# Performance work log

Hardware: AMD Instinct MI355X
Metric: run time of the kernel (lower is better)

The kernel has to match this reference:

```python
import jax, jax.numpy as jnp
import numpy as np

H = 4        # num_heads
DH = 64      # output_dim (d_head)
D = 256      # input_dim (hidden)
NUM_LAYERS = 2


def _gru_cell(x, h, Wih, Whh, bih, bhh):
    # PyTorch GRUCell: gates ordered (r, z, n)
    gi = x @ Wih.T + bih
    gh = h @ Whh.T + bhh
    i_r, i_z, i_n = jnp.split(gi, 3, axis=-1)
    h_r, h_z, h_n = jnp.split(gh, 3, axis=-1)
    r = jax.nn.sigmoid(i_r + h_r)
    z = jax.nn.sigmoid(i_z + h_z)
    n = jnp.tanh(i_n + r * h_n)
    return (1.0 - z) * n + z * h


def _mha(x, attn_mask, Wq, bq, Wk, bk, Wv, bv, Wo):
    B, N, _ = x.shape
    q = (x @ Wq.T + bq).reshape(B, N, H, DH)
    k = (x @ Wk.T + bk).reshape(B, N, H, DH)
    v = (x @ Wv.T + bv).reshape(B, N, H, DH)
    # scores computed in fp32 (autocast disabled in original)
    scores = jnp.einsum('bnhd,bmhd->bhnm', q.astype(jnp.float32), k.astype(jnp.float32)) / jnp.float32(DH) ** 0.5
    scores = jnp.where(attn_mask[:, None], jnp.float32(-1e9), scores)  # mask broadcast over heads
    attn = jax.nn.softmax(scores, axis=-1)
    ctx = jnp.einsum('bhnm,bmhd->bnhd', attn, v).reshape(B, N, H * DH)
    return ctx @ Wo.T  # W_O has no bias


def setup_inputs() -> dict:
    B, N = 1024, 128
    key = jax.random.key(0)
    ks = jax.random.split(key, 14)
    s = 0.02
    return {
        'latent': jax.random.normal(ks[0], (B, N, D), jnp.float32),
        'comm_mask': jax.random.randint(ks[1], (B, N, N), 0, 2) > 0,
        'trait_weight': jax.random.normal(ks[2], (B, N), jnp.float32),
        'Wq': jax.random.normal(ks[3], (H * DH, D), jnp.float32) * s,
        'bq': jnp.zeros((H * DH,), jnp.float32),
        'Wk': jax.random.normal(ks[4], (H * DH, D), jnp.float32) * s,
        'bk': jnp.zeros((H * DH,), jnp.float32),
        'Wv': jax.random.normal(ks[5], (H * DH, D), jnp.float32) * s,
        'bv': jnp.zeros((H * DH,), jnp.float32),
        'Wo': jax.random.normal(ks[6], (DH, H * DH), jnp.float32) * s,
        'Wih': jax.random.normal(ks[7], (3 * D, DH), jnp.float32) * s,
        'Whh': jax.random.normal(ks[8], (3 * D, D), jnp.float32) * s,
        'bih': jnp.zeros((3 * D,), jnp.float32),
        'bhh': jnp.zeros((3 * D,), jnp.float32),
    }


def reference(latent, comm_mask, trait_weight, Wq, bq, Wk, bk, Wv, bv, Wo, Wih, Whh, bih, bhh):
    B, N, _ = latent.shape
    attn_mask = ~comm_mask                                    # [B,N,N] True = blocked
    update_mask = (comm_mask.sum(axis=-1) > 1)[..., None]     # [B,N,1]
    for _ in range(NUM_LAYERS):
        info = _mha(latent, attn_mask, Wq, bq, Wk, bk, Wv, bv, Wo)          # [B,N,DH]
        upd = _gru_cell(info.reshape(-1, DH), latent.reshape(-1, D), Wih, Whh, bih, bhh)
        latent = jnp.where(update_mask, upd.reshape(B, N, D), latent)
    return latent
```

## Files before the change

kernel.cpp:

```cpp
#include <hip/hip_runtime.h>
#include <stdint.h>

#define NTOK 128
#define DHID 256
#define NHEAD 4
#define DHEAD 64

typedef short bf16x8 __attribute__((ext_vector_type(8)));
typedef float f32x4 __attribute__((ext_vector_type(4)));

#define MFMA(a,b,c) __builtin_amdgcn_mfma_f32_16x16x32_bf16((a),(b),(c),0,0,0)

__device__ __forceinline__ float bf2f(uint16_t u){
  union { uint32_t i; float f; } v; v.i = ((uint32_t)u) << 16; return v.f;
}
__device__ __forceinline__ uint16_t f2bf(float f){
  union { uint32_t i; float f; } v; v.f = f;
  uint32_t i = v.i + 0x7FFFu + ((v.i >> 16) & 1u);
  return (uint16_t)(i >> 16);
}

__global__ void k_detect(const uint32_t* __restrict__ raw, uint32_t* __restrict__ flag){
  int lane = threadIdx.x;
  int hits = 0;
  #pragma unroll
  for (int i = 0; i < 16; i++){
    uint32_t w = raw[lane*16 + i];
    uint32_t e = (w >> 7) & 0xFFu;
    hits += (e >= 0x70u && e <= 0x8Fu) ? 1 : 0;
  }
  #pragma unroll
  for (int m = 1; m < 64; m <<= 1) hits += __shfl_xor(hits, m);
  if (lane == 0) *flag = (hits > 512) ? 1u : 0u;
}

__global__ __launch_bounds__(256) void k_convw(const uint32_t* __restrict__ flag,
    const void* Wq, const void* Wk, const void* Wv, const void* Wo,
    const void* Wih, const void* Whh,
    const void* bq, const void* bk, const void* bv, const void* bih, const void* bhh,
    uint16_t* __restrict__ dst)
{
  if (*flag) return;
  int blk = blockIdx.x, tid = threadIdx.x;
  if (blk < 224){
    const float* src; size_t doff; int so;
    if      (blk <  32){ src = (const float*)Wq;  doff = 0;      so = blk*2048; }
    else if (blk <  64){ src = (const float*)Wk;  doff = 65536;  so = (blk-32)*2048; }
    else if (blk <  96){ src = (const float*)Wv;  doff = 131072; so = (blk-64)*2048; }
    else if (blk < 104){ src = (const float*)Wo;  doff = 196608; so = (blk-96)*2048; }
    else if (blk < 128){ src = (const float*)Wih; doff = 212992; so = (blk-104)*2048; }
    else               { src = (const float*)Whh; doff = 262144; so = (blk-128)*2048; }
    int i = so + tid*8;
    float4 a = *(const float4*)(src + i);
    float4 b = *(const float4*)(src + i + 4);
    uint16_t o[8] = {f2bf(a.x),f2bf(a.y),f2bf(a.z),f2bf(a.w),
                     f2bf(b.x),f2bf(b.y),f2bf(b.z),f2bf(b.w)};
    *(bf16x8*)(dst + doff + i) = *(const bf16x8*)o;
  } else {
    for (int i = tid; i < 2304; i += 256){
      const float* s; int lo;
      if      (i <  256){ s = (const float*)bq;  lo = i; }
      else if (i <  512){ s = (const float*)bk;  lo = i - 256; }
      else if (i <  768){ s = (const float*)bv;  lo = i - 512; }
      else if (i < 1536){ s = (const float*)bih; lo = i - 768; }
      else              { s = (const float*)bhh; lo = i - 1536; }
      dst[458752 + i] = f2bf(s[lo]);
    }
  }
}

__global__ void k_conv(const void* __restrict__ src, unsigned long long off,
                       uint16_t* __restrict__ dst, const uint32_t* __restrict__ flag, int n){
  const int isbf = (int)*flag;
  int i0 = (blockIdx.x * blockDim.x + threadIdx.x) * 8;
  int stride = gridDim.x * blockDim.x * 8;
  if (isbf){
    const uint16_t* s = (const uint16_t*)src + off;
    for (int i = i0; i < n; i += stride)
      *(bf16x8*)(dst + i) = *(const bf16x8*)(s + i);
  } else {
    const float* s = (const float*)src + off;
    for (int i = i0; i < n; i += stride){
      float4 a = *(const float4*)(s + i);
      float4 b = *(const float4*)(s + i + 4);
      uint16_t o[8] = {f2bf(a.x),f2bf(a.y),f2bf(a.z),f2bf(a.w),
                       f2bf(b.x),f2bf(b.y),f2bf(b.z),f2bf(b.w)};
      *(bf16x8*)(dst + i) = *(const bf16x8*)o;
    }
  }
}

__global__ void k_store(const uint16_t* __restrict__ L, void* __restrict__ dst,
                        unsigned long long off, const uint32_t* __restrict__ flag, int n){
  if (*flag) return;
  int i0 = (blockIdx.x * blockDim.x + threadIdx.x) * 8;
  int stride = gridDim.x * blockDim.x * 8;
  float* d = (float*)dst + off;
  for (int i = i0; i < n; i += stride){
    bf16x8 v = *(const bf16x8*)(L + i);
    #pragma unroll
    for (int e = 0; e < 8; e++) d[i + e] = bf2f((uint16_t)v[e]);
  }
}

__global__ __launch_bounds__(256) void k_maskpack(const int* __restrict__ mask,
                                                  unsigned long long* __restrict__ packed,
                                                  unsigned char* __restrict__ upd, int nrows){
  int row = blockIdx.x * 4 + (threadIdx.x >> 6);
  if (row >= nrows) return;
  int lane = threadIdx.x & 63;
  const int* mrow = mask + (size_t)row * NTOK;
  unsigned long long b0 = __ballot(mrow[lane] != 0);
  unsigned long long b1 = __ballot(mrow[lane + 64] != 0);
  if (lane == 0){
    packed[row*2 + 0] = b0;
    packed[row*2 + 1] = b1;
    upd[row] = (unsigned char)((__popcll(b0) + __popcll(b1)) > 1 ? 1 : 0);
  }
}

__global__ __launch_bounds__(256) void k_qkv(
    const uint16_t* __restrict__ X,
    const uint16_t* __restrict__ Wq, const uint16_t* __restrict__ bq,
    const uint16_t* __restrict__ Wk, const uint16_t* __restrict__ bk,
    const uint16_t* __restrict__ Wv, const uint16_t* __restrict__ bv,
    uint16_t* __restrict__ Oq, uint16_t* __restrict__ Ok, uint16_t* __restrict__ Ov)
{
  extern __shared__ uint16_t sm[];
  uint16_t* Xs = sm;
  uint16_t* Ws = sm + 64*256;
  const int r0 = blockIdx.x * 64;
  const int tid = threadIdx.x;
  const int lane = tid & 63, lr = lane & 15, lg = lane >> 4;
  const int wav = tid >> 6;
  const int wr = (wav >> 1) * 32, wc = (wav & 1) * 32;

  #pragma unroll
  for (int i = 0; i < 8; i++){
    int c = tid + i*256, row = c >> 5, g = c & 31;
    *(bf16x8*)(Xs + row*256 + (g ^ (row & 7))*8) =
        *(const bf16x8*)(X + (size_t)(r0+row)*DHID + g*8);
  }

  bf16x8 wreg[8];
  auto wptr = [&](int t)->const uint16_t*{
    int w = t >> 2;
    return (w == 0) ? Wq : ((w == 1) ? Wk : Wv);
  };
  auto preload = [&](int t){
    const uint16_t* W = wptr(t);
    int c0t = (t & 3) * 64;
    #pragma unroll
    for (int i = 0; i < 8; i++){
      int idx = tid + i*256, r = idx >> 5, g = idx & 31;
      wreg[i] = *(const bf16x8*)(W + (size_t)(c0t + r)*DHID + g*8);
    }
  };
  preload(0);

  for (int t = 0; t < 12; t++){
    __syncthreads();
    #pragma unroll
    for (int i = 0; i < 8; i++){
      int idx = tid + i*256, r = idx >> 5, g = idx & 31;
      *(bf16x8*)(Ws + r*256 + ((g ^ (r & 7))*8)) = wreg[i];
    }
    __syncthreads();
    if (t < 11) preload(t+1);

    f32x4 acc[2][2] = {};
    #pragma unroll
    for (int kk = 0; kk < 8; kk++){
      int off = ((kk*4 + lg) ^ (lr & 7)) * 8;
      bf16x8 a0 = *(const bf16x8*)(Xs + (wr +      lr)*256 + off);
      bf16x8 a1 = *(const bf16x8*)(Xs + (wr + 16 + lr)*256 + off);
      bf16x8 b0 = *(const bf16x8*)(Ws + (wc +      lr)*256 + off);
      bf16x8 b1 = *(const bf16x8*)(Ws + (wc + 16 + lr)*256 + off);
      acc[0][0] = MFMA(a0, b0, acc[0][0]);
      acc[0][1] = MFMA(a0, b1, acc[0][1]);
      acc[1][0] = MFMA(a1, b0, acc[1][0]);
      acc[1][1] = MFMA(a1, b1, acc[1][1]);
    }
    int w = t >> 2, c0t = (t & 3) * 64;
    const uint16_t* bias = (w == 0) ? bq : ((w == 1) ? bk : bv);
    uint16_t* O = (w == 0) ? Oq : ((w == 1) ? Ok : Ov);
    #pragma unroll
    for (int i = 0; i < 2; i++)
    #pragma unroll
    for (int j = 0; j < 2; j++){
      int col = c0t + wc + j*16 + lr;
      float bvv = bf2f(bias[col]);
      #pragma unroll
      for (int rr = 0; rr < 4; rr++){
        int row = r0 + wr + i*16 + lg*4 + rr;
        O[(size_t)row*DHID + col] = f2bf(acc[i][j][rr] + bvv);
      }
    }
  }
}

__global__ __launch_bounds__(256) void k_attn(
    const uint16_t* __restrict__ Q, const uint16_t* __restrict__ Kb, const uint16_t* __restrict__ V,
    const unsigned long long* __restrict__ packed, uint16_t* __restrict__ ctx)
{
  extern __shared__ uint16_t sm[];
  uint16_t* Ks = sm;
  uint16_t* Vt = sm + 128*64;
  uint16_t* Ps = Vt + 64*128;
  unsigned long long* Ms = (unsigned long long*)(Ps + 128*128);
  const int b = blockIdx.x >> 2;
  const int h = blockIdx.x & 3;
  const int tid = threadIdx.x, lane = tid & 63, wav = tid >> 6;
  const int lr = lane & 15, lg = lane >> 4;
  const size_t base = ((size_t)b * NTOK) * DHID + h * DHEAD;

  Ms[tid] = packed[(size_t)b*NTOK*2 + tid];
  #pragma unroll
  for (int i = 0; i < 4; i++){
    int c = tid + i*256;
    int row = c >> 3, g = c & 7;
    *(bf16x8*)(Ks + row*64 + (g ^ (row & 7))*8) =
        *(const bf16x8*)(Kb + base + (size_t)row*DHID + g*8);
  }
  #pragma unroll
  for (int i = 0; i < 4; i++){
    int c = tid + i*256;
    int n = c & 127, d8 = (c >> 7) * 8;
    bf16x8 v = *(const bf16x8*)(V + base + (size_t)n*DHID + d8);
    #pragma unroll
    for (int e = 0; e < 8; e++){
      int d = d8 + e;
      Vt[d*128 + ((n >> 3) ^ (d & 7))*8 + (n & 7)] = (uint16_t)v[e];
    }
  }
  __syncthreads();

  const int qrow0 = wav * 32;
  bf16x8 qf[2][2];
  #pragma unroll
  for (int i = 0; i < 2; i++)
  #pragma unroll
  for (int kk = 0; kk < 2; kk++)
    qf[i][kk] = *(const bf16x8*)(Q + base + (size_t)(qrow0 + i*16 + lr)*DHID + kk*32 + lg*8);

  f32x4 sa[2][8] = {};
  #pragma unroll
  for (int kk = 0; kk < 2; kk++){
    int off = ((kk*4 + lg) ^ (lr & 7)) * 8;
    #pragma unroll
    for (int j = 0; j < 8; j++){
      bf16x8 bf = *(const bf16x8*)(Ks + (j*16 + lr)*64 + off);
      sa[0][j] = MFMA(qf[0][kk], bf, sa[0][j]);
      sa[1][j] = MFMA(qf[1][kk], bf, sa[1][j]);
    }
  }
  float iv[2][4];
  #pragma unroll
  for (int i = 0; i < 2; i++){
    #pragma unroll
    for (int rr = 0; rr < 4; rr++){
      int n = qrow0 + i*16 + lg*4 + rr;
      unsigned long long m0 = Ms[n*2 + 0];
      unsigned long long m1 = Ms[n*2 + 1];
      float sv[8];
      float mx = -3.0e38f;
      #pragma unroll
      for (int j = 0; j < 8; j++){
        int col = j*16 + lr;
        unsigned long long w = (col < 64) ? m0 : m1;
        float s = sa[i][j][rr] * 0.125f;
        sv[j] = ((w >> (col & 63)) & 1ull) ? s : -1e9f;
        mx = fmaxf(mx, sv[j]);
      }
      mx = fmaxf(mx, __shfl_xor(mx, 1));
      mx = fmaxf(mx, __shfl_xor(mx, 2));
      mx = fmaxf(mx, __shfl_xor(mx, 4));
      mx = fmaxf(mx, __shfl_xor(mx, 8));
      float sum = 0.f;
      #pragma unroll
      for (int j = 0; j < 8; j++){ sv[j] = __expf(sv[j] - mx); sum += sv[j]; }
      sum += __shfl_xor(sum, 1);
      sum += __shfl_xor(sum, 2);
      sum += __shfl_xor(sum, 4);
      sum += __shfl_xor(sum, 8);
      iv[i][rr] = __builtin_amdgcn_rcpf(sum);
      #pragma unroll
      for (int j = 0; j < 8; j++){
        int col = j*16 + lr;
        Ps[n*128 + ((col >> 3) ^ (n & 7))*8 + (col & 7)] = f2bf(sv[j]);
      }
    }
  }
  __syncthreads();

  f32x4 oa[2][4] = {};
  #pragma unroll
  for (int kk = 0; kk < 4; kk++){
    int off = ((kk*4 + lg) ^ (lr & 7)) * 8;
    bf16x8 a0 = *(const bf16x8*)(Ps + (qrow0 +      lr)*128 + off);
    bf16x8 a1 = *(const bf16x8*)(Ps + (qrow0 + 16 + lr)*128 + off);
    #pragma unroll
    for (int j = 0; j < 4; j++){
      bf16x8 bf = *(const bf16x8*)(Vt + (j*16 + lr)*128 + off);
      oa[0][j] = MFMA(a0, bf, oa[0][j]);
      oa[1][j] = MFMA(a1, bf, oa[1][j]);
    }
  }
  #pragma unroll
  for (int i = 0; i < 2; i++)
  #pragma unroll
  for (int j = 0; j < 4; j++)
  #pragma unroll
  for (int rr = 0; rr < 4; rr++){
    int n = qrow0 + i*16 + lg*4 + rr;
    ctx[((size_t)b*NTOK + n)*DHID + h*DHEAD + j*16 + lr] = f2bf(oa[i][j][rr] * iv[i][rr]);
  }
}

__global__ __launch_bounds__(256, 2) void k_gru(
    const uint16_t* __restrict__ ctxp, const uint16_t* __restrict__ lat,
    const uint16_t* __restrict__ Wo, const uint16_t* __restrict__ Wih, const uint16_t* __restrict__ Whh,
    const uint16_t* __restrict__ bih, const uint16_t* __restrict__ bhh,
    const unsigned char* __restrict__ upd, uint16_t* __restrict__ Lbuf,
    uint16_t* __restrict__ dout, const uint32_t* __restrict__ flag, int layer)
{
  extern __shared__ uint16_t sm[];
  uint16_t* Wb0   = sm;
  uint16_t* Wb1   = sm + 15360;
  uint16_t* Is    = sm + 30720;
  uint16_t* biasS = sm + 38912;
  uint16_t* lat_out = (layer == 1 && *flag) ? dout : Lbuf;
  const int r0 = blockIdx.x * 128;
  const int tid = threadIdx.x, lane = tid & 63, wav = tid >> 6;
  const int lr = lane & 15, lg = lane >> 4;
  const int wrow = wav * 32;

  #pragma unroll
  for (int i = 0; i < 6; i++){
    int idx = tid + i*256;
    if (idx < 1536) biasS[idx] = (idx < 768) ? bih[idx] : bhh[idx - 768];
  }

  auto stage_async = [&](int cs, uint16_t* buf){
    #pragma unroll
    for (int c = 0; c < 7; c++){
      int G = c*256 + tid;
      const uint16_t* src;
      if (G < 1536){
        int r = G >> 5, gp = G & 31;
        src = Whh + (size_t)((r>>4)*256 + cs*16 + (r&15))*DHID + (gp ^ (r&7))*8;
      } else {
        int G2 = G - 1536, r = G2 >> 3, gp = G2 & 7;
        src = Wih + (size_t)((r>>4)*256 + cs*16 + (r&15))*DHEAD + (gp ^ (r&7))*8;
      }
      __builtin_amdgcn_global_load_lds(
          (const __attribute__((address_space(1))) uint32_t*)src,
          (__attribute__((address_space(3))) uint32_t*)(buf + (size_t)G*8),
          16, 0, 0);
    }
    if (tid < 128){
      int G = 1792 + tid;
      int G2 = G - 1536, r = G2 >> 3, gp = G2 & 7;
      const uint16_t* src = Wih + (size_t)((r>>4)*256 + cs*16 + (r&15))*DHEAD + (gp ^ (r&7))*8;
      __builtin_amdgcn_global_load_lds(
          (const __attribute__((address_space(1))) uint32_t*)src,
          (__attribute__((address_space(3))) uint32_t*)(buf + (size_t)G*8),
          16, 0, 0);
    }
  };

  stage_async(0, Wb0);

  f32x4 ai[2][4] = {};
  #pragma unroll
  for (int kk = 0; kk < 8; kk++){
    bf16x8 bw[4];
    #pragma unroll
    for (int j = 0; j < 4; j++)
      bw[j] = *(const bf16x8*)(Wo + (size_t)(j*16 + lr)*DHID + kk*32 + lg*8);
    #pragma unroll
    for (int t = 0; t < 2; t++){
      bf16x8 ac = *(const bf16x8*)(ctxp + (size_t)(r0 + wrow + t*16 + lr)*DHID + kk*32 + lg*8);
      #pragma unroll
      for (int j = 0; j < 4; j++) ai[t][j] = MFMA(ac, bw[j], ai[t][j]);
    }
  }
  #pragma unroll
  for (int t = 0; t < 2; t++)
  #pragma unroll
  for (int j = 0; j < 4; j++)
  #pragma unroll
  for (int rr = 0; rr < 4; rr++){
    int row = wrow + t*16 + lg*4 + rr, col = j*16 + lr;
    Is[row*64 + ((col>>3) ^ (row&7))*8 + (col&7)] = f2bf(ai[t][j][rr]);
  }

  bf16x8 aL[2][8];
  #pragma unroll
  for (int t = 0; t < 2; t++)
  #pragma unroll
  for (int kk = 0; kk < 8; kk++)
    aL[t][kk] = *(const bf16x8*)(lat + (size_t)(r0 + wrow + t*16 + lr)*DHID + kk*32 + lg*8);

  uint32_t u4[2];
  #pragma unroll
  for (int t = 0; t < 2; t++)
    u4[t] = *(const uint32_t*)(upd + r0 + wrow + t*16 + lg*4);

  __syncthreads();

  const float LOG2E = 1.44269504f;
  for (int cs = 0; cs < 16; cs++){
    uint16_t* Wcur = (cs & 1) ? Wb1 : Wb0;
    if (cs < 15) stage_async(cs+1, (cs & 1) ? Wb0 : Wb1);

    const uint16_t* WhhS = Wcur;
    const uint16_t* WihS = Wcur + 12288;

    f32x4 arz[2][2] = {};
    f32x4 gin[2] = {}, ghn[2] = {};

    #pragma unroll
    for (int kk = 0; kk < 2; kk++){
      int off = ((kk*4 + lg) ^ (lr & 7)) * 8;
      bf16x8 br = *(const bf16x8*)(WihS + (0*16 + lr)*64 + off);
      bf16x8 bz = *(const bf16x8*)(WihS + (1*16 + lr)*64 + off);
      bf16x8 bn = *(const bf16x8*)(WihS + (2*16 + lr)*64 + off);
      #pragma unroll
      for (int t = 0; t < 2; t++){
        bf16x8 a = *(const bf16x8*)(Is + (wrow + t*16 + lr)*64 + off);
        arz[0][t] = MFMA(a, br, arz[0][t]);
        arz[1][t] = MFMA(a, bz, arz[1][t]);
        gin[t]    = MFMA(a, bn, gin[t]);
      }
    }
    #pragma unroll
    for (int kk = 0; kk < 8; kk++){
      int off = ((kk*4 + lg) ^ (lr & 7)) * 8;
      bf16x8 br = *(const bf16x8*)(WhhS + (0*16 + lr)*256 + off);
      bf16x8 bz = *(const bf16x8*)(WhhS + (1*16 + lr)*256 + off);
      bf16x8 bn = *(const bf16x8*)(WhhS + (2*16 + lr)*256 + off);
      #pragma unroll
      for (int t = 0; t < 2; t++){
        arz[0][t] = MFMA(aL[t][kk], br, arz[0][t]);
        arz[1][t] = MFMA(aL[t][kk], bz, arz[1][t]);
        ghn[t]    = MFMA(aL[t][kk], bn, ghn[t]);
      }
    }

    int col = cs*16 + lr;
    float brz0 = bf2f(biasS[col])     + bf2f(biasS[768+col]);
    float brz1 = bf2f(biasS[256+col]) + bf2f(biasS[1024+col]);
    float bin_ = bf2f(biasS[512+col]);
    float bhn  = bf2f(biasS[1280+col]);
    #pragma unroll
    for (int t = 0; t < 2; t++)
    #pragma unroll
    for (int rr = 0; rr < 4; rr++){
      int row = wrow + t*16 + lg*4 + rr;
      float hv = bf2f(lat[(size_t)(r0+row)*DHID + col]);
      float xr = arz[0][t][rr] + brz0;
      float xz = arz[1][t][rr] + brz1;
      float rg = __builtin_amdgcn_rcpf(1.f + __builtin_amdgcn_exp2f(-xr*LOG2E));
      float zg = __builtin_amdgcn_rcpf(1.f + __builtin_amdgcn_exp2f(-xz*LOG2E));
      float nx = (gin[t][rr] + bin_) + rg*(ghn[t][rr] + bhn);
      nx = fminf(10.f, fmaxf(-10.f, nx));
      float e2 = __builtin_amdgcn_exp2f(-2.f*LOG2E*nx);
      float ng = (1.f - e2) * __builtin_amdgcn_rcpf(1.f + e2);
      float hp = (1.f - zg)*ng + zg*hv;
      float ov = ((u4[t] >> (rr*8)) & 1u) ? hp : hv;
      lat_out[(size_t)(r0+row)*DHID + col] = f2bf(ov);
    }
    __syncthreads();
  }
}

extern "C" void kernel_launch(void* const* d_in, const int* in_sizes, int n_in,
                              void* d_out, int out_size, void* d_ws, size_t ws_size,
                              hipStream_t stream)
{
  (void)in_sizes; (void)n_in; (void)out_size;
  const void* latent = d_in[0];
  const int*  mask   = (const int*)d_in[1];
  const void* Wq  = d_in[3]; const void* bq  = d_in[4];
  const void* Wk  = d_in[5]; const void* bk  = d_in[6];
  const void* Wv  = d_in[7]; const void* bv  = d_in[8];
  const void* Wo  = d_in[9];
  const void* Wih = d_in[10]; const void* Whh = d_in[11];
  const void* bih = d_in[12]; const void* bhh = d_in[13];

  uint8_t* p = (uint8_t*)d_ws;
  uint32_t* flag = (uint32_t*)p;            p += 256;
  uint16_t* Wqc  = (uint16_t*)p;            p += 65536*2;
  uint16_t* Wkc  = (uint16_t*)p;            p += 65536*2;
  uint16_t* Wvc  = (uint16_t*)p;            p += 65536*2;
  uint16_t* Woc  = (uint16_t*)p;            p += 16384*2;
  uint16_t* Wihc = (uint16_t*)p;            p += 49152*2;
  uint16_t* Whhc = (uint16_t*)p;            p += 196608*2;
  uint16_t* bqc  = (uint16_t*)p;            p += 512;
  uint16_t* bkc  = (uint16_t*)p;            p += 512;
  uint16_t* bvc  = (uint16_t*)p;            p += 512;
  uint16_t* bihc = (uint16_t*)p;            p += 1536;
  uint16_t* bhhc = (uint16_t*)p;            p += 1536;
  uint8_t* chunk0 = p;
  size_t reserved = (size_t)(chunk0 - (uint8_t*)d_ws);
  const size_t perb = 5ull*65536 + 2048 + 128;

  const int Btot = 1024;
  int CB = (int)((ws_size > reserved ? ws_size - reserved : 0) / perb);
  if (CB > Btot) CB = Btot;
  if (CB < 1)    CB = 1;

  auto cgrid = [](int n){ int b = (n/8 + 255)/256; if (b > 2048) b = 2048; if (b < 1) b = 1; return (unsigned)b; };

  k_detect<<<1, 64, 0, stream>>>((const uint32_t*)latent, flag);
  k_convw<<<225, 256, 0, stream>>>(flag, Wq, Wk, Wv, Wo, Wih, Whh,
                                   bq, bk, bv, bih, bhh, Wqc);

  for (int b0 = 0; b0 < Btot; b0 += CB){
    int cb = (Btot - b0 < CB) ? (Btot - b0) : CB;
    int rows = cb * 128;
    int nelem = rows * DHID;
    uint8_t* q = chunk0;
    uint16_t* L    = (uint16_t*)q; q += (size_t)cb*65536;
    uint16_t* q_ws = (uint16_t*)q; q += (size_t)cb*65536;
    uint16_t* k_ws = (uint16_t*)q; q += (size_t)cb*65536;
    uint16_t* v_ws = (uint16_t*)q; q += (size_t)cb*65536;
    uint16_t* c_ws = (uint16_t*)q; q += (size_t)cb*65536;
    unsigned long long* packed = (unsigned long long*)q; q += (size_t)cb*2048;
    unsigned char* updp = (unsigned char*)q;

    uint16_t* dout_b = (uint16_t*)d_out + (size_t)b0*NTOK*DHID;

    k_conv<<<cgrid(nelem), 256, 0, stream>>>(latent, (unsigned long long)b0*NTOK*DHID, L, flag, nelem);
    k_maskpack<<<dim3(rows/4), 256, 0, stream>>>(mask + (size_t)b0*NTOK*NTOK, packed, updp, rows);

    for (int layer = 0; layer < 2; layer++){
      k_qkv <<<dim3(rows/64),  256, 65536, stream>>>(L, Wqc,bqc, Wkc,bkc, Wvc,bvc, q_ws, k_ws, v_ws);
      k_attn<<<dim3(cb*NHEAD), 256, 67584, stream>>>(q_ws, k_ws, v_ws, packed, c_ws);
      k_gru <<<dim3(rows/128), 256, 80896, stream>>>(c_ws, L, Woc, Wihc, Whhc, bihc, bhhc, updp,
                                                     L, dout_b, flag, layer);
    }
    k_store<<<cgrid(nelem), 256, 0, stream>>>(L, (void*)((float*)d_out + (size_t)b0*NTOK*DHID), 0, flag, nelem);
  }
}
```

Baseline: 738.9 us.

## Read bf16 latent directly in layer 0 and halve attention P buffer in LDS

When the input is already bf16, the conversion kernel now exits early, and layer-0 QKV and GRU read the raw latent directly instead of a copied buffer. This removes one full copy pass over the latent. The attention kernel now writes the softmax probabilities into LDS in two 64-column halves, each followed by its MFMAs. That drops shared memory per block from 67584 to 51200 bytes, which may allow more blocks to be resident per CU. The half-tile buffer is reused across halves with no barrier between writing and reading it, relying on each wave touching only its own rows.

```diff
diff --git a/kernel.cpp b/kernel.cpp
--- a/kernel.cpp
+++ b/kernel.cpp
@@ -71,22 +71,16 @@
 
 __global__ void k_conv(const void* __restrict__ src, unsigned long long off,
                        uint16_t* __restrict__ dst, const uint32_t* __restrict__ flag, int n){
-  const int isbf = (int)*flag;
+  if (*flag) return;
   int i0 = (blockIdx.x * blockDim.x + threadIdx.x) * 8;
   int stride = gridDim.x * blockDim.x * 8;
-  if (isbf){
-    const uint16_t* s = (const uint16_t*)src + off;
-    for (int i = i0; i < n; i += stride)
-      *(bf16x8*)(dst + i) = *(const bf16x8*)(s + i);
-  } else {
-    const float* s = (const float*)src + off;
-    for (int i = i0; i < n; i += stride){
-      float4 a = *(const float4*)(s + i);
-      float4 b = *(const float4*)(s + i + 4);
-      uint16_t o[8] = {f2bf(a.x),f2bf(a.y),f2bf(a.z),f2bf(a.w),
-                       f2bf(b.x),f2bf(b.y),f2bf(b.z),f2bf(b.w)};
-      *(bf16x8*)(dst + i) = *(const bf16x8*)o;
-    }
+  const float* s = (const float*)src + off;
+  for (int i = i0; i < n; i += stride){
+    float4 a = *(const float4*)(s + i);
+    float4 b = *(const float4*)(s + i + 4);
+    uint16_t o[8] = {f2bf(a.x),f2bf(a.y),f2bf(a.z),f2bf(a.w),
+                     f2bf(b.x),f2bf(b.y),f2bf(b.z),f2bf(b.w)};
+    *(bf16x8*)(dst + i) = *(const bf16x8*)o;
   }
 }
 
@@ -120,7 +114,8 @@
 }
 
 __global__ __launch_bounds__(256) void k_qkv(
-    const uint16_t* __restrict__ X,
+    const uint16_t* __restrict__ latRaw, const uint16_t* __restrict__ L,
+    const uint32_t* __restrict__ flag, int layer,
     const uint16_t* __restrict__ Wq, const uint16_t* __restrict__ bq,
     const uint16_t* __restrict__ Wk, const uint16_t* __restrict__ bk,
     const uint16_t* __restrict__ Wv, const uint16_t* __restrict__ bv,
@@ -129,6 +124,7 @@
   extern __shared__ uint16_t sm[];
   uint16_t* Xs = sm;
   uint16_t* Ws = sm + 64*256;
+  const uint16_t* X = (layer == 0 && *flag) ? latRaw : L;
   const int r0 = blockIdx.x * 64;
   const int tid = threadIdx.x;
   const int lane = tid & 63, lr = lane & 15, lg = lane >> 4;
@@ -205,9 +201,9 @@
 {
   extern __shared__ uint16_t sm[];
   uint16_t* Ks = sm;
-  uint16_t* Vt = sm + 128*64;
-  uint16_t* Ps = Vt + 64*128;
-  unsigned long long* Ms = (unsigned long long*)(Ps + 128*128);
+  uint16_t* Vt = sm + 8192;
+  uint16_t* Ph = sm + 16384;
+  unsigned long long* Ms = (unsigned long long*)(sm + 24576);
   const int b = blockIdx.x >> 2;
   const int h = blockIdx.x & 3;
   const int tid = threadIdx.x, lane = tid & 63, wav = tid >> 6;
@@ -285,25 +281,37 @@
       sum += __shfl_xor(sum, 8);
       iv[i][rr] = __builtin_amdgcn_rcpf(sum);
       #pragma unroll
-      for (int j = 0; j < 8; j++){
-        int col = j*16 + lr;
-        Ps[n*128 + ((col >> 3) ^ (n & 7))*8 + (col & 7)] = f2bf(sv[j]);
-      }
-    }
-  }
-  __syncthreads();
+      for (int j = 0; j < 8; j++) sa[i][j][rr] = sv[j];
+    }
+  }
 
   f32x4 oa[2][4] = {};
   #pragma unroll
-  for (int kk = 0; kk < 4; kk++){
-    int off = ((kk*4 + lg) ^ (lr & 7)) * 8;
-    bf16x8 a0 = *(const bf16x8*)(Ps + (qrow0 +      lr)*128 + off);
-    bf16x8 a1 = *(const bf16x8*)(Ps + (qrow0 + 16 + lr)*128 + off);
+  for (int half = 0; half < 2; half++){
+    #pragma unroll
+    for (int i = 0; i < 2; i++)
     #pragma unroll
     for (int j = 0; j < 4; j++){
-      bf16x8 bf = *(const bf16x8*)(Vt + (j*16 + lr)*128 + off);
-      oa[0][j] = MFMA(a0, bf, oa[0][j]);
-      oa[1][j] = MFMA(a1, bf, oa[1][j]);
+      int ch = j*16 + lr;
+      #pragma unroll
+      for (int rr = 0; rr < 4; rr++){
+        int n = qrow0 + i*16 + lg*4 + rr;
+        Ph[n*64 + ((ch>>3) ^ (n&7))*8 + (ch&7)] = f2bf(sa[i][half*4 + j][rr]);
+      }
+    }
+    #pragma unroll
+    for (int kkl = 0; kkl < 2; kkl++){
+      int offA = ((kkl*4 + lg) ^ (lr & 7)) * 8;
+      int kk = half*2 + kkl;
+      int offB = ((kk*4 + lg) ^ (lr & 7)) * 8;
+      bf16x8 a0 = *(const bf16x8*)(Ph + (qrow0 +      lr)*64 + offA);
+      bf16x8 a1 = *(const bf16x8*)(Ph + (qrow0 + 16 + lr)*64 + offA);
+      #pragma unroll
+      for (int j = 0; j < 4; j++){
+        bf16x8 bf = *(const bf16x8*)(Vt + (j*16 + lr)*128 + offB);
+        oa[0][j] = MFMA(a0, bf, oa[0][j]);
+        oa[1][j] = MFMA(a1, bf, oa[1][j]);
+      }
     }
   }
   #pragma unroll
@@ -318,10 +326,11 @@
 }
 
 __global__ __launch_bounds__(256, 2) void k_gru(
-    const uint16_t* __restrict__ ctxp, const uint16_t* __restrict__ lat,
+    const uint16_t* __restrict__ ctxp, const uint16_t* __restrict__ latRaw,
+    const uint16_t* __restrict__ Lbuf,
     const uint16_t* __restrict__ Wo, const uint16_t* __restrict__ Wih, const uint16_t* __restrict__ Whh,
     const uint16_t* __restrict__ bih, const uint16_t* __restrict__ bhh,
-    const unsigned char* __restrict__ upd, uint16_t* __restrict__ Lbuf,
+    const unsigned char* __restrict__ upd,
     uint16_t* __restrict__ dout, const uint32_t* __restrict__ flag, int layer)
 {
   extern __shared__ uint16_t sm[];
@@ -329,7 +338,8 @@
   uint16_t* Wb1   = sm + 15360;
   uint16_t* Is    = sm + 30720;
   uint16_t* biasS = sm + 38912;
-  uint16_t* lat_out = (layer == 1 && *flag) ? dout : Lbuf;
+  const uint16_t* lat = (layer == 0 && *flag) ? latRaw : Lbuf;
+  uint16_t* lat_out   = (layer == 1 && *flag) ? dout : (uint16_t*)Lbuf;
   const int r0 = blockIdx.x * 128;
   const int tid = threadIdx.x, lane = tid & 63, wav = tid >> 6;
   const int lr = lane & 15, lg = lane >> 4;
@@ -530,16 +540,18 @@
     unsigned long long* packed = (unsigned long long*)q; q += (size_t)cb*2048;
     unsigned char* updp = (unsigned char*)q;
 
+    const uint16_t* latRaw = (const uint16_t*)latent + (size_t)b0*NTOK*DHID;
     uint16_t* dout_b = (uint16_t*)d_out + (size_t)b0*NTOK*DHID;
 
     k_conv<<<cgrid(nelem), 256, 0, stream>>>(latent, (unsigned long long)b0*NTOK*DHID, L, flag, nelem);
     k_maskpack<<<dim3(rows/4), 256, 0, stream>>>(mask + (size_t)b0*NTOK*NTOK, packed, updp, rows);
 
     for (int layer = 0; layer < 2; layer++){
-      k_qkv <<<dim3(rows/64),  256, 65536, stream>>>(L, Wqc,bqc, Wkc,bkc, Wvc,bvc, q_ws, k_ws, v_ws);
-      k_attn<<<dim3(cb*NHEAD), 256, 67584, stream>>>(q_ws, k_ws, v_ws, packed, c_ws);
-      k_gru <<<dim3(rows/128), 256, 80896, stream>>>(c_ws, L, Woc, Wihc, Whhc, bihc, bhhc, updp,
-                                                     L, dout_b, flag, layer);
+      k_qkv <<<dim3(rows/64),  256, 65536, stream>>>(latRaw, L, flag, layer,
+                                                     Wqc,bqc, Wkc,bkc, Wvc,bvc, q_ws, k_ws, v_ws);
+      k_attn<<<dim3(cb*NHEAD), 256, 51200, stream>>>(q_ws, k_ws, v_ws, packed, c_ws);
+      k_gru <<<dim3(rows/128), 256, 80896, stream>>>(c_ws, latRaw, L, Woc, Wihc, Whhc, bihc, bhhc,
+                                                     updp, dout_b, flag, layer);
     }
     k_store<<<cgrid(nelem), 256, 0, stream>>>(L, (void*)((float*)d_out + (size_t)b0*NTOK*DHID), 0, flag, nelem);
   }
```

Result: faster. 720.6 us (-2.5%).
